# Optimization experiments

Hardware: AMD Instinct MI355X
Metric: run time of the kernel (lower is better)

Reference implementation:

```python
import jax, jax.numpy as jnp
import numpy as np
from jax import lax

F_CNT = 64    # factories per player
U_CNT = 2048  # units per player
GRID = 16     # spatial map side after stride-3 conv on 48x48 board


def conv2d(x, w, b, stride=1, pad=1):
    return lax.conv_general_dilated(x, w, (stride, stride), [(pad, pad), (pad, pad)],
                                    dimension_numbers=('NCHW', 'OIHW', 'NCHW')) + b[None, :, None, None]


def prelu(x, a):
    return jnp.where(x > 0, x, a * x)


def linear(x, w, b):
    return x @ w.T + b


def layernorm(x, g, b, eps=1e-5):
    mu = jnp.mean(x, -1, keepdims=True)
    var = jnp.mean((x - mu) ** 2, -1, keepdims=True)
    return (x - mu) / jnp.sqrt(var + eps) * g + b


def maxpool2(x):
    return lax.reduce_window(x, -jnp.inf, lax.max, (1, 1, 2, 2), (1, 1, 2, 2), 'VALID')


def mha4(f0, u0, f1, u1, fw, fb, uw, ub, lw, lb, num_heads=2, hidden=32):
    # FourSequenceMHAttention: per head, per player, separate Q/K/V linears for
    # factories and units; sequence order is [fac_p0, units_p0, fac_p1, units_p1].
    scale = hidden ** 0.5
    heads = []
    for h in range(num_heads):
        Q, K, V = [], [], []
        for i, (f, u) in enumerate(((f0, u0), (f1, u1))):
            b0 = h * 6 + i * 3
            Q.append(linear(f, fw[b0], fb[b0]))
            K.append(linear(f, fw[b0 + 1], fb[b0 + 1]))
            V.append(linear(f, fw[b0 + 2], fb[b0 + 2]))
            Q.append(linear(u, uw[b0], ub[b0]))
            K.append(linear(u, uw[b0 + 1], ub[b0 + 1]))
            V.append(linear(u, uw[b0 + 2], ub[b0 + 2]))
        Qc = jnp.concatenate(Q, 1)
        Kc = jnp.concatenate(K, 1)
        Vc = jnp.concatenate(V, 1)
        attn = jax.nn.softmax(jnp.einsum('bqd,bkd->bqk', Qc, Kc) / scale, axis=-1)
        heads.append(jnp.einsum('bqk,bkd->bqd', attn, Vc))
    return linear(jnp.concatenate(heads, -1), lw, lb)


def scatter_mask(feat, pos, C):
    # one-hot scatter-add of per-unit features onto the 16x16 grid (batch==1)
    gm = jnp.zeros((GRID, GRID, C), feat.dtype).at[pos[:, 0], pos[:, 1]].add(feat[0])
    return jnp.transpose(gm, (2, 0, 1))[None]  # [1,C,16,16]


def _forward(fl, p0_fac_pos, p0_unit_pos, p1_fac_pos, p1_unit_pos):
    (board, p0_fac_feat, p0_unit_feat, p1_fac_feat, p1_unit_feat,
     sp_w1, sp_b1, sp_a1, sp_w2, sp_b2, sp_a2, sp_w3, sp_b3,
     enc_fac_w, enc_fac_b, enc_unit_w, enc_unit_b, enc_lin_w, enc_lin_b,
     ext_fac_w, ext_fac_b, ext_unit_w, ext_unit_b, ext_lin_w, ext_lin_b, ext_ln_g, ext_ln_b,
     v_w1, v_b1, v_a1, v_w2, v_b2, v_a2, v_lw, v_lb,
     fo_w1, fo_b1, fo_a, fo_w2, fo_b2, ro_w1, ro_b1, ro_a, ro_w2, ro_b2) = fl

    sm = prelu(conv2d(board, sp_w1, sp_b1), sp_a1)
    sm = prelu(conv2d(sm, sp_w2, sp_b2), sp_a2)
    sm = conv2d(sm, sp_w3, sp_b3, stride=3, pad=0)  # [1,24,16,16]

    def gather(pos):
        # per-unit gather of the 24-dim spatial feature at (pos_x, pos_y)
        return jnp.transpose(sm[0][:, pos[:, 0], pos[:, 1]], (1, 0))[None]  # [1,N,24]

    f0 = jnp.concatenate([p0_fac_feat, gather(p0_fac_pos)], -1)    # [1,F,31]
    u0 = jnp.concatenate([p0_unit_feat, gather(p0_unit_pos)], -1)  # [1,U,38]
    f1 = jnp.concatenate([p1_fac_feat, gather(p1_fac_pos)], -1)
    u1 = jnp.concatenate([p1_unit_feat, gather(p1_unit_pos)], -1)

    gmu0 = scatter_mask(p0_unit_feat, p0_unit_pos, 14)
    gmf0 = scatter_mask(p0_fac_feat, p0_fac_pos, 7)
    gmu1 = scatter_mask(p1_unit_feat, p1_unit_pos, 14)
    gmf1 = scatter_mask(p1_fac_feat, p1_fac_pos, 7)
    # loop prepends each team's masks: after p1 order is [u1, f1, u0, f0, spatial]
    v_map = jnp.concatenate([gmu1, gmf1, gmu0, gmf0, sm], 1)  # [1,66,16,16]

    seq = mha4(f0, u0, f1, u1, enc_fac_w, enc_fac_b, enc_unit_w, enc_unit_b, enc_lin_w, enc_lin_b)
    S0, S1, S2 = F_CNT, F_CNT + U_CNT, 2 * F_CNT + U_CNT
    for l in range(2):
        new = mha4(seq[:, :S0], seq[:, S0:S1], seq[:, S1:S2], seq[:, S2:],
                   ext_fac_w[l], ext_fac_b[l], ext_unit_w[l], ext_unit_b[l],
                   ext_lin_w[l], ext_lin_b[l])
        seq = layernorm(seq + new, ext_ln_g[l], ext_ln_b[l])

    def head2(x, w1, b1, a, w2, b2):
        return linear(prelu(linear(x, w1, b1), a), w2, b2)

    f0o = head2(seq[:, :S0], fo_w1, fo_b1, fo_a, fo_w2, fo_b2)      # [1,F,4]
    u0o = head2(seq[:, S0:S1], ro_w1, ro_b1, ro_a, ro_w2, ro_b2)    # [1,U,17]
    f1o = head2(seq[:, S1:S2], fo_w1, fo_b1, fo_a, fo_w2, fo_b2)
    u1o = head2(seq[:, S2:], ro_w1, ro_b1, ro_a, ro_w2, ro_b2)

    vm = maxpool2(prelu(conv2d(v_map, v_w1, v_b1), v_a1))  # [1,96,8,8]
    vm = maxpool2(prelu(conv2d(vm, v_w2, v_b2), v_a2))     # [1,128,4,4]
    v = jnp.tanh(vm.reshape(vm.shape[0], -1) @ v_lw.T + v_lb)  # [1,1]
    return (f0o, u0o, f1o, u1o, v)


def setup_inputs() -> dict:
    key = jax.random.key(0)
    ks = iter(jax.random.split(key, 64))

    def rn(shape, s=1.0):
        return s * jax.random.normal(next(ks), shape, dtype=jnp.float32)

    def ri(shape):
        return jax.random.randint(next(ks), shape, 0, GRID)

    a25 = lambda: jnp.full((1,), 0.25, jnp.float32)  # torch PReLU default
    inp = {
        'board': rn((1, 14, 48, 48)),
        'p0_fac_feat': rn((1, F_CNT, 7)), 'p0_unit_feat': rn((1, U_CNT, 14)),
        'p1_fac_feat': rn((1, F_CNT, 7)), 'p1_unit_feat': rn((1, U_CNT, 14)),
        'sp_w1': rn((48, 14, 3, 3), 0.05), 'sp_b1': rn((48,), 0.05), 'sp_a1': a25(),
        'sp_w2': rn((96, 48, 3, 3), 0.05), 'sp_b2': rn((96,), 0.05), 'sp_a2': a25(),
        'sp_w3': rn((24, 96, 3, 3), 0.05), 'sp_b3': rn((24,), 0.05),
        'enc_fac_w': rn((12, 32, 31), 0.05), 'enc_fac_b': rn((12, 32), 0.05),
        'enc_unit_w': rn((12, 32, 38), 0.05), 'enc_unit_b': rn((12, 32), 0.05),
        'enc_lin_w': rn((32, 64), 0.05), 'enc_lin_b': rn((32,), 0.05),
        'ext_fac_w': rn((2, 12, 32, 32), 0.05), 'ext_fac_b': rn((2, 12, 32), 0.05),
        'ext_unit_w': rn((2, 12, 32, 32), 0.05), 'ext_unit_b': rn((2, 12, 32), 0.05),
        'ext_lin_w': rn((2, 32, 64), 0.05), 'ext_lin_b': rn((2, 32), 0.05),
        'ext_ln_g': jnp.ones((2, 32), jnp.float32), 'ext_ln_b': jnp.zeros((2, 32), jnp.float32),
        'v_w1': rn((96, 66, 3, 3), 0.05), 'v_b1': rn((96,), 0.05), 'v_a1': a25(),
        'v_w2': rn((128, 96, 3, 3), 0.05), 'v_b2': rn((128,), 0.05), 'v_a2': a25(),
        'v_lw': rn((1, 128 * 16), 0.05), 'v_lb': rn((1,), 0.05),
        'fo_w1': rn((32, 32), 0.05), 'fo_b1': rn((32,), 0.05), 'fo_a': a25(),
        'fo_w2': rn((4, 32), 0.05), 'fo_b2': rn((4,), 0.05),
        'ro_w1': rn((32, 32), 0.05), 'ro_b1': rn((32,), 0.05), 'ro_a': a25(),
        'ro_w2': rn((17, 32), 0.05), 'ro_b2': rn((17,), 0.05),
        'p0_fac_pos': ri((F_CNT, 2)), 'p0_unit_pos': ri((U_CNT, 2)),
        'p1_fac_pos': ri((F_CNT, 2)), 'p1_unit_pos': ri((U_CNT, 2)),
    }
    return inp


def reference(board, p0_fac_feat, p0_unit_feat, p1_fac_feat, p1_unit_feat,
              sp_w1, sp_b1, sp_a1, sp_w2, sp_b2, sp_a2, sp_w3, sp_b3,
              enc_fac_w, enc_fac_b, enc_unit_w, enc_unit_b, enc_lin_w, enc_lin_b,
              ext_fac_w, ext_fac_b, ext_unit_w, ext_unit_b, ext_lin_w, ext_lin_b, ext_ln_g, ext_ln_b,
              v_w1, v_b1, v_a1, v_w2, v_b2, v_a2, v_lw, v_lb,
              fo_w1, fo_b1, fo_a, fo_w2, fo_b2, ro_w1, ro_b1, ro_a, ro_w2, ro_b2,
              p0_fac_pos, p0_unit_pos, p1_fac_pos, p1_unit_pos):
    fl = (board, p0_fac_feat, p0_unit_feat, p1_fac_feat, p1_unit_feat,
          sp_w1, sp_b1, sp_a1, sp_w2, sp_b2, sp_a2, sp_w3, sp_b3,
          enc_fac_w, enc_fac_b, enc_unit_w, enc_unit_b, enc_lin_w, enc_lin_b,
          ext_fac_w, ext_fac_b, ext_unit_w, ext_unit_b, ext_lin_w, ext_lin_b, ext_ln_g, ext_ln_b,
          v_w1, v_b1, v_a1, v_w2, v_b2, v_a2, v_lw, v_lb,
          fo_w1, fo_b1, fo_a, fo_w2, fo_b2, ro_w1, ro_b1, ro_a, ro_w2, ro_b2)
    return _forward(fl, p0_fac_pos, p0_unit_pos, p1_fac_pos, p1_unit_pos)
```

## Files before the change

### kernel.cpp

```cpp
#include <hip/hip_runtime.h>
#include <hip/hip_bf16.h>

#define SEQ 4224
typedef unsigned int uint;
typedef unsigned short ushort;
typedef __attribute__((ext_vector_type(8))) short bf16x8;
typedef __attribute__((ext_vector_type(4))) float f32x4;

__device__ __forceinline__ float prelu_f(float x, float a){ return x > 0.f ? x : a*x; }

__device__ __forceinline__ ushort bfr(float x){
  uint u = __float_as_uint(x);
  u = (u + 0x7fffu + ((u>>16)&1u)) >> 16;
  return (ushort)u;
}
__device__ __forceinline__ uint pkbf(float a, float b){
  __hip_bfloat162 h2 = __float22bfloat162_rn(make_float2(a,b));
  union { __hip_bfloat162 h; uint u; } cv; cv.h = h2; return cv.u;
}

#define QSCALE 0.25505607190037247f

template<int CIN, int COUT, int HW, int ACT, int CPT>
__global__ __launch_bounds__(256) void conv3x3_v2(const float* __restrict__ in, const float* __restrict__ w,
                          const float* __restrict__ bias, const float* __restrict__ alpha,
                          float* __restrict__ out) {
  __shared__ float Ws[CPT*CIN*9];
  __shared__ float Bs[CPT];
  const int PXB = HW*HW/256;
  int cg = blockIdx.x / PXB, pxb = blockIdx.x % PXB;
  int tid = threadIdx.x;
  for (int idx=tid; idx<CPT*CIN*9; idx+=256) Ws[idx] = w[cg*CPT*CIN*9 + idx];
  if (tid<CPT) Bs[tid] = bias[cg*CPT+tid];
  __syncthreads();
  int p = pxb*256 + tid;
  int x = p % HW, y = p / HW;
  float a = ACT ? alpha[0] : 0.f;
  float acc[CPT];
  #pragma unroll
  for (int c=0;c<CPT;++c) acc[c]=Bs[c];
  #pragma unroll 2
  for (int i=0;i<CIN;++i){
    const float* ip = in + i*HW*HW;
    float win[9];
    #pragma unroll
    for (int ky=0;ky<3;++ky){
      int yy = y+ky-1;
      #pragma unroll
      for (int kx=0;kx<3;++kx){
        int xx = x+kx-1;
        bool ok = ((unsigned)yy < (unsigned)HW) && ((unsigned)xx < (unsigned)HW);
        win[ky*3+kx] = ok ? ip[yy*HW+xx] : 0.f;
      }
    }
    #pragma unroll
    for (int c=0;c<CPT;++c){
      const float* wp = &Ws[(c*CIN+i)*9];
      #pragma unroll
      for (int k=0;k<9;++k) acc[c] += win[k]*wp[k];
    }
  }
  #pragma unroll
  for (int c=0;c<CPT;++c){
    float v = acc[c];
    if (ACT) v = prelu_f(v, a);
    out[(cg*CPT+c)*HW*HW + p] = v;
  }
}

__global__ __launch_bounds__(256) void conv_s3_v2(const float* __restrict__ in, const float* __restrict__ w,
                        const float* __restrict__ bias, float* __restrict__ out) {
  __shared__ float Ws[2*96*9];
  int cg = blockIdx.x;
  int tid = threadIdx.x;
  for (int idx=tid; idx<1728; idx+=256) Ws[idx] = w[cg*1728 + idx];
  __syncthreads();
  int x = tid&15, y = tid>>4;
  float a0 = bias[2*cg], a1 = bias[2*cg+1];
  const float* ip0 = in + y*144 + x*3;
  #pragma unroll 4
  for (int i=0;i<96;++i){
    const float* ip = ip0 + i*2304;
    float win[9];
    #pragma unroll
    for (int ky=0;ky<3;++ky)
      #pragma unroll
      for (int kx=0;kx<3;++kx) win[ky*3+kx] = ip[ky*48+kx];
    const float* w0 = &Ws[i*9];
    const float* w1 = &Ws[864 + i*9];
    #pragma unroll
    for (int k=0;k<9;++k){ a0 += win[k]*w0[k]; a1 += win[k]*w1[k]; }
  }
  out[(2*cg)*256 + y*16 + x] = a0;
  out[(2*cg+1)*256 + y*16 + x] = a1;
}

__global__ __launch_bounds__(256) void gather_concat(const float* __restrict__ sm,
  const float* __restrict__ p0f, const float* __restrict__ p0u,
  const float* __restrict__ p1f, const float* __restrict__ p1u,
  const int* __restrict__ p0fp, const int* __restrict__ p0up,
  const int* __restrict__ p1fp, const int* __restrict__ p1up,
  float* __restrict__ F0, float* __restrict__ U0, float* __restrict__ F1, float* __restrict__ U1)
{
  int e = blockIdx.x*256+threadIdx.x;
  if (e>=SEQ) return;
  const float* feat; const int* pos; float* dst; int nf, n;
  if (e<64){ n=e; feat=p0f+n*7; pos=p0fp; dst=F0+n*31; nf=7; }
  else if (e<2112){ n=e-64; feat=p0u+n*14; pos=p0up; dst=U0+(size_t)n*38; nf=14; }
  else if (e<2176){ n=e-2112; feat=p1f+n*7; pos=p1fp; dst=F1+n*31; nf=7; }
  else { n=e-2176; feat=p1u+n*14; pos=p1up; dst=U1+(size_t)n*38; nf=14; }
  for (int c=0;c<nf;++c) dst[c]=feat[c];
  int px = pos[2*n], py = pos[2*n+1];
  const float* s = sm + px*16 + py;
  #pragma unroll
  for (int c=0;c<24;++c) dst[nf+c] = s[c*256];
}

__global__ __launch_bounds__(256) void vmap_init(const float* __restrict__ sm, float* __restrict__ vmap){
  int t = blockIdx.x*256+threadIdx.x;
  if (t>=66*256) return;
  int c = t>>8;
  vmap[t] = (c<42)? 0.f : sm[t - 42*256];
}

__global__ __launch_bounds__(256) void vmap_scatter(
  const float* __restrict__ p0f, const float* __restrict__ p0u,
  const float* __restrict__ p1f, const float* __restrict__ p1u,
  const int* __restrict__ p0fp, const int* __restrict__ p0up,
  const int* __restrict__ p1fp, const int* __restrict__ p1up,
  float* __restrict__ vmap)
{
  int e = blockIdx.x*256+threadIdx.x;
  if (e>=SEQ) return;
  const float* feat; const int* pos; int n, ch0, C;
  if (e<2048){ n=e; feat=p1u+n*14; pos=p1up; ch0=0; C=14; }
  else if (e<2112){ n=e-2048; feat=p1f+n*7; pos=p1fp; ch0=14; C=7; }
  else if (e<4160){ n=e-2112; feat=p0u+n*14; pos=p0up; ch0=21; C=14; }
  else { n=e-4160; feat=p0f+n*7; pos=p0fp; ch0=35; C=7; }
  int off = pos[2*n]*16 + pos[2*n+1];
  for (int c=0;c<C;++c) atomicAdd(&vmap[(ch0+c)*256 + off], feat[c]);
}

__global__ __launch_bounds__(256) void qkv_proj2(const float* __restrict__ x0, const float* __restrict__ x1,
    const float* __restrict__ x2, const float* __restrict__ x3, int ind_f, int ind_u,
    const float* __restrict__ fw, const float* __restrict__ fb,
    const float* __restrict__ uw, const float* __restrict__ ub,
    ushort* __restrict__ Q16, ushort* __restrict__ K16, ushort* __restrict__ VT16){
  __shared__ float Xs[64*40];
  __shared__ float Ws[32*40];
  __shared__ float Bs[32];
  int blk = blockIdx.x;
  int chunk = blk % 66;
  int hm = blk / 66;
  int m = hm >> 1, h = hm & 1;
  const float* xb; int ind, isfac, pl;
  if (chunk==0){ xb=x0; ind=ind_f; isfac=1; pl=0; }
  else if (chunk<=32){ xb=x1 + (size_t)(chunk-1)*64*ind_u; ind=ind_u; isfac=0; pl=0; }
  else if (chunk==33){ xb=x2; ind=ind_f; isfac=1; pl=1; }
  else { xb=x3 + (size_t)(chunk-34)*64*ind_u; ind=ind_u; isfac=0; pl=1; }
  int b0 = h*6 + pl*3 + m;
  const float* w = (isfac? fw:uw) + (size_t)b0*32*ind;
  const float* bias = (isfac? fb:ub) + b0*32;
  int tid = threadIdx.x;
  {
    int r = tid>>2, seg = tid&3;
    const float* xr = xb + (size_t)r*ind;
    #pragma unroll
    for (int j=0;j<10;++j){
      int c = seg*10+j;
      Xs[r*40+c] = (c<ind) ? xr[c] : 0.f;
    }
    int o = tid>>3, sg = tid&7;
    const float* wr = w + (size_t)o*ind;
    #pragma unroll
    for (int j=0;j<5;++j){
      int c = sg*5+j;
      Ws[o*40+c] = (c<ind) ? wr[c] : 0.f;
    }
    if (tid<32) Bs[tid]=bias[tid];
  }
  __syncthreads();
  int og = tid&7, rg = tid>>3;
  const float4* Xs4 = (const float4*)Xs;
  const float4* Ws4 = (const float4*)Ws;
  float acc[2][4];
  #pragma unroll
  for (int k=0;k<4;++k){ float b = Bs[og+8*k]; acc[0][k]=b; acc[1][k]=b; }
  #pragma unroll
  for (int d4=0; d4<10; ++d4){
    float4 xa = Xs4[rg*10+d4];
    float4 xb2 = Xs4[(rg+32)*10+d4];
    #pragma unroll
    for (int k=0;k<4;++k){
      float4 wv = Ws4[(og+8*k)*10+d4];
      acc[0][k] += xa.x*wv.x + xa.y*wv.y + xa.z*wv.z + xa.w*wv.w;
      acc[1][k] += xb2.x*wv.x + xb2.y*wv.y + xb2.z*wv.z + xb2.w*wv.w;
    }
  }
  if (m==0){
    #pragma unroll
    for (int j=0;j<2;++j){
      int r = rg + 32*j;
      ushort* base = Q16 + ((size_t)h*SEQ + chunk*64 + r)*32;
      #pragma unroll
      for (int k=0;k<4;++k) base[og+8*k] = bfr(acc[j][k]*QSCALE);
    }
  } else if (m==1){
    #pragma unroll
    for (int j=0;j<2;++j){
      int r = rg + 32*j;
      ushort* base = K16 + ((size_t)h*SEQ + chunk*64 + r)*32;
      #pragma unroll
      for (int k=0;k<4;++k) base[og+8*k] = bfr(acc[j][k]);
    }
  } else {
    #pragma unroll
    for (int k=0;k<4;++k){
      ushort* base = VT16 + ((size_t)h*32 + og+8*k)*SEQ + chunk*64;
      #pragma unroll
      for (int j=0;j<2;++j) base[rg+32*j] = bfr(acc[j][k]);
    }
  }
}

#define KSPLIT 6
#define KITERS 11
__global__ __launch_bounds__(256) void flash_mfma(const ushort* __restrict__ Q16,
    const ushort* __restrict__ K16, const ushort* __restrict__ VT16,
    float* __restrict__ Hpart, float* __restrict__ aux){
  __shared__ ushort Ks[2][64][40];
  __shared__ ushort VTs[2][32][80];
  __shared__ ushort Pl[4][16][72];
  int qb = blockIdx.x, h = blockIdx.y, ks = blockIdx.z;
  int tid = threadIdx.x;
  int wv = tid>>6, l = tid&63, lq = l&15, g = l>>4;
  const ushort* Qh = Q16 + (size_t)h*SEQ*32;
  const ushort* Kh = K16 + (size_t)h*SEQ*32;
  const ushort* VTh = VT16 + (size_t)h*32*SEQ;

  bf16x8 qf = *(const bf16x8*)(Qh + (size_t)(qb*64 + wv*16 + lq)*32 + g*8);

  int krow = tid>>2, kc8 = (tid&3)*8;
  int vd = tid>>3, vk8 = (tid&7)*8;

  f32x4 o0 = {0.f,0.f,0.f,0.f}, o1 = {0.f,0.f,0.f,0.f};
  float mr = -1e30f, lrow = 0.f;

  int kt0 = ks*KITERS;
  bf16x8 kpre = *(const bf16x8*)(Kh + (size_t)(kt0*64 + krow)*32 + kc8);
  bf16x8 vpre = *(const bf16x8*)(VTh + (size_t)vd*SEQ + kt0*64 + vk8);
  *(bf16x8*)&Ks[0][krow][kc8] = kpre;
  *(bf16x8*)&VTs[0][vd][vk8] = vpre;

  for (int it=0; it<KITERS; ++it){
    int pb = it&1;
    if (it+1 < KITERS){
      kpre = *(const bf16x8*)(Kh + (size_t)((kt0+it+1)*64 + krow)*32 + kc8);
      vpre = *(const bf16x8*)(VTh + (size_t)vd*SEQ + (kt0+it+1)*64 + vk8);
    }
    __syncthreads();
    f32x4 z = {0.f,0.f,0.f,0.f};
    f32x4 sT[4];
    #pragma unroll
    for (int m=0;m<4;++m){
      bf16x8 kf = *(const bf16x8*)&Ks[pb][16*m + lq][g*8];
      sT[m] = __builtin_amdgcn_mfma_f32_16x16x32_bf16(kf, qf, z, 0, 0, 0);
    }
    float tm = -1e30f;
    #pragma unroll
    for (int m=0;m<4;++m)
      tm = fmaxf(tm, fmaxf(fmaxf(sT[m][0],sT[m][1]), fmaxf(sT[m][2],sT[m][3])));
    tm = fmaxf(tm, __shfl_xor(tm,16));
    tm = fmaxf(tm, __shfl_xor(tm,32));
    float mnew = fmaxf(mr, tm);
    float rsc = exp2f(mr - mnew);
    float ts = 0.f;
    #pragma unroll
    for (int m=0;m<4;++m){
      #pragma unroll
      for (int r=0;r<4;++r){ float p = exp2f(sT[m][r]-mnew); sT[m][r]=p; ts+=p; }
    }
    ts += __shfl_xor(ts,16); ts += __shfl_xor(ts,32);
    lrow = lrow*rsc + ts; mr = mnew;
    #pragma unroll
    for (int m=0;m<4;++m){
      uint2 pw; pw.x = pkbf(sT[m][0],sT[m][1]); pw.y = pkbf(sT[m][2],sT[m][3]);
      *(uint2*)&Pl[wv][lq][16*m + g*4] = pw;
    }
    float rr0 = __shfl(rsc, (g<<2)+0);
    float rr1 = __shfl(rsc, (g<<2)+1);
    float rr2 = __shfl(rsc, (g<<2)+2);
    float rr3 = __shfl(rsc, (g<<2)+3);
    o0[0]*=rr0; o0[1]*=rr1; o0[2]*=rr2; o0[3]*=rr3;
    o1[0]*=rr0; o1[1]*=rr1; o1[2]*=rr2; o1[3]*=rr3;
    #pragma unroll
    for (int s=0;s<2;++s){
      bf16x8 pf = *(const bf16x8*)&Pl[wv][lq][s*32 + g*8];
      bf16x8 vf0 = *(const bf16x8*)&VTs[pb][lq][s*32 + g*8];
      bf16x8 vf1 = *(const bf16x8*)&VTs[pb][lq+16][s*32 + g*8];
      o0 = __builtin_amdgcn_mfma_f32_16x16x32_bf16(pf, vf0, o0, 0, 0, 0);
      o1 = __builtin_amdgcn_mfma_f32_16x16x32_bf16(pf, vf1, o1, 0, 0, 0);
    }
    if (it+1 < KITERS){
      *(bf16x8*)&Ks[pb^1][krow][kc8] = kpre;
      *(bf16x8*)&VTs[pb^1][vd][vk8] = vpre;
    }
  }
  int qg0 = qb*64 + wv*16;
  #pragma unroll
  for (int r=0;r<4;++r){
    size_t row = (size_t)ks*SEQ + qg0 + g*4 + r;
    Hpart[row*64 + h*32 + lq]      = o0[r];
    Hpart[row*64 + h*32 + lq + 16] = o1[r];
  }
  if (g==0){
    float* ap = aux + ((size_t)(ks*2+h)*SEQ + qg0 + lq)*2;
    ap[0]=mr; ap[1]=lrow;
  }
}

__device__ __forceinline__ float combine_row(const float* __restrict__ Hp,
    const float* __restrict__ aux, int s, int d){
  int hh = d>>5;
  float m[KSPLIT], li[KSPLIT];
  #pragma unroll
  for (int p=0;p<KSPLIT;++p){
    const float* ap = aux + ((size_t)(p*2+hh)*SEQ + s)*2;
    m[p]=ap[0]; li[p]=ap[1];
  }
  float ms = m[0];
  #pragma unroll
  for (int p=1;p<KSPLIT;++p) ms = fmaxf(ms, m[p]);
  float den = 0.f, hv = 0.f;
  #pragma unroll
  for (int p=0;p<KSPLIT;++p){
    float w = exp2f(m[p]-ms);
    den += li[p]*w;
    hv  += Hp[(size_t)p*SEQ*64 + (size_t)s*64 + d]*w;
  }
  return hv/den;
}

__global__ __launch_bounds__(256) void outlin_enc3(const float* __restrict__ Hp,
     const float* __restrict__ aux, const float* __restrict__ lw,
     const float* __restrict__ lb, float* __restrict__ seqout){
  __shared__ float Ls[32*68];
  __shared__ float Hc[8*68];
  int tid=threadIdx.x;
  int s0 = blockIdx.x*8;
  for (int idx=tid; idx<2048; idx+=256){ int o=idx>>6, d=idx&63; Ls[o*68+d]=lw[idx]; }
  for (int idx=tid; idx<512; idx+=256){
    int sl = idx>>6, d = idx&63;
    Hc[sl*68+d] = combine_row(Hp, aux, s0+sl, d);
  }
  __syncthreads();
  int o = tid&31, sl = tid>>5;
  const float4* H4 = (const float4*)&Hc[sl*68];
  const float4* L4 = (const float4*)&Ls[o*68];
  float acc = lb[o];
  #pragma unroll
  for (int d4=0; d4<16; ++d4){
    float4 hv = H4[d4], lv = L4[d4];
    acc += hv.x*lv.x + hv.y*lv.y + hv.z*lv.z + hv.w*lv.w;
  }
  seqout[(s0+sl)*32+o]=acc;
}

__global__ __launch_bounds__(256) void outlin_ln3(const float* __restrict__ Hp,
    const float* __restrict__ aux, const float* __restrict__ lw,
    const float* __restrict__ lb, const float* __restrict__ seqin,
    const float* __restrict__ g, const float* __restrict__ b, float* __restrict__ seqout){
  __shared__ float Ls[32*68];
  __shared__ float Hc[8*68];
  int tid=threadIdx.x;
  int s0 = blockIdx.x*8;
  for (int idx=tid; idx<2048; idx+=256){ int o=idx>>6, d=idx&63; Ls[o*68+d]=lw[idx]; }
  for (int idx=tid; idx<512; idx+=256){
    int sl = idx>>6, d = idx&63;
    Hc[sl*68+d] = combine_row(Hp, aux, s0+sl, d);
  }
  __syncthreads();
  int o = tid&31, sl = tid>>5;
  const float4* H4 = (const float4*)&Hc[sl*68];
  const float4* L4 = (const float4*)&Ls[o*68];
  float acc = lb[o] + seqin[(s0+sl)*32+o];
  #pragma unroll
  for (int d4=0; d4<16; ++d4){
    float4 hv = H4[d4], lv = L4[d4];
    acc += hv.x*lv.x + hv.y*lv.y + hv.z*lv.z + hv.w*lv.w;
  }
  float sum=acc;
  #pragma unroll
  for (int off=1; off<32; off<<=1) sum += __shfl_xor(sum,off);
  float mu = sum*0.03125f;
  float dv = acc-mu;
  float vs = dv*dv;
  #pragma unroll
  for (int off=1; off<32; off<<=1) vs += __shfl_xor(vs,off);
  float rstd = rsqrtf(vs*0.03125f + 1e-5f);
  seqout[(s0+sl)*32+o] = dv*rstd*g[o] + b[o];
}

__global__ __launch_bounds__(256) void head_mlp(const float* __restrict__ seq,
  const float* __restrict__ fw1,const float* __restrict__ fb1,const float* __restrict__ fa,
  const float* __restrict__ fw2,const float* __restrict__ fb2,
  const float* __restrict__ rw1,const float* __restrict__ rb1,const float* __restrict__ ra,
  const float* __restrict__ rw2,const float* __restrict__ rb2,
  float* __restrict__ out)
{
  int e = blockIdx.x*256+threadIdx.x;
  if (e>=SEQ) return;
  const float *w1,*b1,*w2,*b2; float a; int od; float* dst;
  if (e<64){ w1=fw1;b1=fb1;a=fa[0];w2=fw2;b2=fb2;od=4; dst=out + e*4; }
  else if (e<2112){ w1=rw1;b1=rb1;a=ra[0];w2=rw2;b2=rb2;od=17; dst=out + 256 + (size_t)(e-64)*17; }
  else if (e<2176){ w1=fw1;b1=fb1;a=fa[0];w2=fw2;b2=fb2;od=4; dst=out + 35072 + (e-2112)*4; }
  else { w1=rw1;b1=rb1;a=ra[0];w2=rw2;b2=rb2;od=17; dst=out + 35328 + (size_t)(e-2176)*17; }
  float x[32];
  #pragma unroll
  for (int i=0;i<32;++i) x[i]=seq[(size_t)e*32+i];
  float hbuf[32];
  #pragma unroll
  for (int j=0;j<32;++j){
    float acc=b1[j];
    #pragma unroll
    for (int i=0;i<32;++i) acc+=w1[j*32+i]*x[i];
    hbuf[j]=prelu_f(acc,a);
  }
  for (int k=0;k<od;++k){
    float acc=b2[k];
    #pragma unroll
    for (int j=0;j<32;++j) acc+=w2[k*32+j]*hbuf[j];
    dst[k]=acc;
  }
}

__global__ __launch_bounds__(128) void vconv1_pool(const float* __restrict__ in, const float* __restrict__ w,
    const float* __restrict__ bias, const float* __restrict__ alpha, float* __restrict__ out){
  __shared__ float In[66*160];
  __shared__ float Wc[594];
  int c = blockIdx.x >> 1, half = blockIdx.x & 1;
  int y0 = half*8;
  int tid = threadIdx.x;
  const float4* in4 = (const float4*)in;
  float4* In4 = (float4*)In;
  for (int idx4=tid; idx4<2640; idx4+=128){
    int i = idx4/40, rem = idx4 - i*40;
    int r = rem>>2, x4 = rem&3;
    int y = y0 - 1 + r;
    float4 v;
    if ((unsigned)y < 16u) v = in4[i*64 + y*4 + x4];
    else { v.x=v.y=v.z=v.w=0.f; }
    In4[idx4] = v;
  }
  for (int idx=tid; idx<594; idx+=128) Wc[idx] = w[c*594 + idx];
  __syncthreads();
  int x = tid & 15, ry = tid >> 4;
  float a = alpha[0];
  float acc = bias[c];
  for (int i=0;i<66;++i){
    const float* base = &In[i*160 + ry*16];
    const float* wp = &Wc[i*9];
    #pragma unroll
    for (int ky=0;ky<3;++ky){
      const float* row = base + ky*16;
      #pragma unroll
      for (int kx=0;kx<3;++kx){
        int xx = x+kx-1;
        float v = ((unsigned)xx<16u) ? row[xx] : 0.f;
        acc += v*wp[ky*3+kx];
      }
    }
  }
  acc = prelu_f(acc, a);
  float mx = fmaxf(acc, __shfl_xor(acc,1));
  mx = fmaxf(mx, __shfl_xor(mx,16));
  if (((x&1)==0) && ((ry&1)==0))
    out[c*64 + (half*4 + (ry>>1))*8 + (x>>1)] = mx;
}

__global__ __launch_bounds__(64) void vconv2_pool(const float* __restrict__ in, const float* __restrict__ w,
    const float* __restrict__ bias, const float* __restrict__ alpha, float* __restrict__ out){
  __shared__ float In[96*64];
  __shared__ float Ws[864];
  int c = blockIdx.x;
  int tid = threadIdx.x;
  const float4* in4 = (const float4*)in;
  float4* In4 = (float4*)In;
  for (int idx4=tid; idx4<1536; idx4+=64) In4[idx4] = in4[idx4];
  for (int idx=tid; idx<864; idx+=64) Ws[idx] = w[c*864 + idx];
  __syncthreads();
  int x = tid&7, y = tid>>3;
  float acc = bias[c];
  for (int i=0;i<96;++i){
    const float* base = &In[i*64];
    const float* wp = &Ws[i*9];
    #pragma unroll
    for (int ky=0;ky<3;++ky){
      int yy = y+ky-1;
      #pragma unroll
      for (int kx=0;kx<3;++kx){
        int xx = x+kx-1;
        bool ok = ((unsigned)yy<8u) && ((unsigned)xx<8u);
        float v = ok ? base[yy*8+xx] : 0.f;
        acc += v*wp[ky*3+kx];
      }
    }
  }
  acc = prelu_f(acc, alpha[0]);
  float mx = fmaxf(acc, __shfl_xor(acc,1));
  mx = fmaxf(mx, __shfl_xor(mx,8));
  if (((x&1)==0) && ((y&1)==0))
    out[c*16 + (y>>1)*4 + (x>>1)] = mx;
}

__global__ __launch_bounds__(256) void vfinal(const float* __restrict__ vp2, const float* __restrict__ lw,
                       const float* __restrict__ lb, float* __restrict__ outv){
  __shared__ float red[256];
  int tid=threadIdx.x;
  float s=0.f;
  for (int i=tid;i<2048;i+=256) s += vp2[i]*lw[i];
  red[tid]=s; __syncthreads();
  for (int k=128;k>0;k>>=1){ if (tid<k) red[tid]+=red[tid+k]; __syncthreads(); }
  if (tid==0) outv[0] = tanhf(red[0]+lb[0]);
}

extern "C" void kernel_launch(void* const* d_in, const int* in_sizes, int n_in,
                              void* d_out, int out_size, void* d_ws, size_t ws_size,
                              hipStream_t stream){
  (void)in_sizes; (void)n_in; (void)out_size; (void)ws_size;
  const float* board = (const float*)d_in[0];
  const float* p0f = (const float*)d_in[1];
  const float* p0u = (const float*)d_in[2];
  const float* p1f = (const float*)d_in[3];
  const float* p1u = (const float*)d_in[4];
  const float* sp_w1=(const float*)d_in[5];  const float* sp_b1=(const float*)d_in[6];  const float* sp_a1=(const float*)d_in[7];
  const float* sp_w2=(const float*)d_in[8];  const float* sp_b2=(const float*)d_in[9];  const float* sp_a2=(const float*)d_in[10];
  const float* sp_w3=(const float*)d_in[11]; const float* sp_b3=(const float*)d_in[12];
  const float* enc_fac_w=(const float*)d_in[13]; const float* enc_fac_b=(const float*)d_in[14];
  const float* enc_unit_w=(const float*)d_in[15]; const float* enc_unit_b=(const float*)d_in[16];
  const float* enc_lin_w=(const float*)d_in[17]; const float* enc_lin_b=(const float*)d_in[18];
  const float* ext_fac_w=(const float*)d_in[19]; const float* ext_fac_b=(const float*)d_in[20];
  const float* ext_unit_w=(const float*)d_in[21]; const float* ext_unit_b=(const float*)d_in[22];
  const float* ext_lin_w=(const float*)d_in[23]; const float* ext_lin_b=(const float*)d_in[24];
  const float* ext_ln_g=(const float*)d_in[25]; const float* ext_ln_b=(const float*)d_in[26];
  const float* v_w1=(const float*)d_in[27]; const float* v_b1=(const float*)d_in[28]; const float* v_a1=(const float*)d_in[29];
  const float* v_w2=(const float*)d_in[30]; const float* v_b2=(const float*)d_in[31]; const float* v_a2=(const float*)d_in[32];
  const float* v_lw=(const float*)d_in[33]; const float* v_lb=(const float*)d_in[34];
  const float* fo_w1=(const float*)d_in[35]; const float* fo_b1=(const float*)d_in[36]; const float* fo_a=(const float*)d_in[37];
  const float* fo_w2=(const float*)d_in[38]; const float* fo_b2=(const float*)d_in[39];
  const float* ro_w1=(const float*)d_in[40]; const float* ro_b1=(const float*)d_in[41]; const float* ro_a=(const float*)d_in[42];
  const float* ro_w2=(const float*)d_in[43]; const float* ro_b2=(const float*)d_in[44];
  const int* p0fp=(const int*)d_in[45]; const int* p0up=(const int*)d_in[46];
  const int* p1fp=(const int*)d_in[47]; const int* p1up=(const int*)d_in[48];
  float* out = (float*)d_out;

  float* W = (float*)d_ws;
  float* sm1 = W;
  float* sm2 = sm1 + 110592;
  float* sm  = sm2 + 221184;
  float* F0  = sm + 6144;
  float* U0  = F0 + 1984;
  float* F1  = U0 + 77824;
  float* U1  = F1 + 1984;
  ushort* q16 = (ushort*)(U1 + 77824);
  ushort* k16 = q16 + 2*SEQ*32;
  ushort* vt16 = k16 + 2*SEQ*32;
  float* Hp  = (float*)(vt16 + 2*SEQ*32);
  float* aux = Hp + KSPLIT*SEQ*64;
  float* seqA= aux + KSPLIT*2*SEQ*2;
  float* seqB= seqA + SEQ*32;
  float* vmap= seqB + SEQ*32;
  float* vp1 = vmap + 66*256;
  float* vp2 = vp1 + 96*64;

  conv3x3_v2<14,48,48,1,4><<<108,256,0,stream>>>(board, sp_w1, sp_b1, sp_a1, sm1);
  conv3x3_v2<48,96,48,1,4><<<216,256,0,stream>>>(sm1, sp_w2, sp_b2, sp_a2, sm2);
  conv_s3_v2<<<12,256,0,stream>>>(sm2, sp_w3, sp_b3, sm);
  gather_concat<<<17,256,0,stream>>>(sm, p0f,p0u,p1f,p1u, p0fp,p0up,p1fp,p1up, F0,U0,F1,U1);
  vmap_init<<<66,256,0,stream>>>(sm, vmap);
  vmap_scatter<<<17,256,0,stream>>>(p0f,p0u,p1f,p1u, p0fp,p0up,p1fp,p1up, vmap);
  vconv1_pool<<<192,128,0,stream>>>(vmap, v_w1, v_b1, v_a1, vp1);
  vconv2_pool<<<128,64,0,stream>>>(vp1, v_w2, v_b2, v_a2, vp2);
  vfinal<<<1,256,0,stream>>>(vp2, v_lw, v_lb, out + 70144);

  qkv_proj2<<<396,256,0,stream>>>(F0,U0,F1,U1, 31,38, enc_fac_w,enc_fac_b,enc_unit_w,enc_unit_b, q16,k16,vt16);
  flash_mfma<<<dim3(66,2,KSPLIT),256,0,stream>>>(q16,k16,vt16,Hp,aux);
  outlin_enc3<<<528,256,0,stream>>>(Hp, aux, enc_lin_w, enc_lin_b, seqA);
  qkv_proj2<<<396,256,0,stream>>>(seqA, seqA+64*32, seqA+2112*32, seqA+2176*32, 32,32,
      ext_fac_w, ext_fac_b, ext_unit_w, ext_unit_b, q16,k16,vt16);
  flash_mfma<<<dim3(66,2,KSPLIT),256,0,stream>>>(q16,k16,vt16,Hp,aux);
  outlin_ln3<<<528,256,0,stream>>>(Hp, aux, ext_lin_w, ext_lin_b, seqA, ext_ln_g, ext_ln_b, seqB);
  qkv_proj2<<<396,256,0,stream>>>(seqB, seqB+64*32, seqB+2112*32, seqB+2176*32, 32,32,
      ext_fac_w+12288, ext_fac_b+384, ext_unit_w+12288, ext_unit_b+384, q16,k16,vt16);
  flash_mfma<<<dim3(66,2,KSPLIT),256,0,stream>>>(q16,k16,vt16,Hp,aux);
  outlin_ln3<<<528,256,0,stream>>>(Hp, aux, ext_lin_w+2048, ext_lin_b+32, seqB, ext_ln_g+32, ext_ln_b+32, seqA);

  head_mlp<<<17,256,0,stream>>>(seqA, fo_w1,fo_b1,fo_a,fo_w2,fo_b2, ro_w1,ro_b1,ro_a,ro_w2,ro_b2, out);
}
```

Baseline: 405.1 us.

## Fuse whole forward pass into one cooperative persistent megakernel with grid syncs

Replaces the chain of about 19 separate kernel launches with a single cooperative kernel of 512 persistent blocks. The blocks walk every stage as work items and separate stages with grid-wide barriers, so per-launch overhead and inter-kernel gaps go away. The attention key split also changes from 6 to 11 chunks (KITERS 11 to 6), giving more flash work items but more partials to combine. If the cooperative launch fails, it falls back to launching the per-stage kernels separately. Risks are grid-sync cost, occupancy limits from the shared-memory union, and load imbalance on small stages.

New measurement: 1.121 ms. 177% more time.

```diff
diff --git a/kernel.cpp b/kernel.cpp
--- a/kernel.cpp
+++ b/kernel.cpp
@@ -1,7 +1,13 @@
 #include <hip/hip_runtime.h>
 #include <hip/hip_bf16.h>
+#include <hip/hip_cooperative_groups.h>
+
+namespace cg = cooperative_groups;
 
 #define SEQ 4224
+#define KSPLIT 11
+#define KITERS 6
+#define NBLK 512
 typedef unsigned int uint;
 typedef unsigned short ushort;
 typedef __attribute__((ext_vector_type(8))) short bf16x8;
@@ -21,24 +27,36 @@
 
 #define QSCALE 0.25505607190037247f
 
-template<int CIN, int COUT, int HW, int ACT, int CPT>
-__global__ __launch_bounds__(256) void conv3x3_v2(const float* __restrict__ in, const float* __restrict__ w,
-                          const float* __restrict__ bias, const float* __restrict__ alpha,
-                          float* __restrict__ out) {
-  __shared__ float Ws[CPT*CIN*9];
-  __shared__ float Bs[CPT];
-  const int PXB = HW*HW/256;
-  int cg = blockIdx.x / PXB, pxb = blockIdx.x % PXB;
-  int tid = threadIdx.x;
-  for (int idx=tid; idx<CPT*CIN*9; idx+=256) Ws[idx] = w[cg*CPT*CIN*9 + idx];
-  if (tid<CPT) Bs[tid] = bias[cg*CPT+tid];
+struct MegaParams {
+  const float *board,*p0f,*p0u,*p1f,*p1u;
+  const float *sp_w1,*sp_b1,*sp_a1,*sp_w2,*sp_b2,*sp_a2,*sp_w3,*sp_b3;
+  const float *enc_fac_w,*enc_fac_b,*enc_unit_w,*enc_unit_b,*enc_lin_w,*enc_lin_b;
+  const float *ext_fac_w,*ext_fac_b,*ext_unit_w,*ext_unit_b,*ext_lin_w,*ext_lin_b,*ext_ln_g,*ext_ln_b;
+  const float *v_w1,*v_b1,*v_a1,*v_w2,*v_b2,*v_a2,*v_lw,*v_lb;
+  const float *fo_w1,*fo_b1,*fo_a,*fo_w2,*fo_b2,*ro_w1,*ro_b1,*ro_a,*ro_w2,*ro_b2;
+  const int *p0fp,*p0up,*p1fp,*p1up;
+  float* out;
+  float *sm1,*sm2,*sm,*F0,*U0,*F1,*U1;
+  ushort *q16,*k16,*vt16;
+  float *Hp,*aux,*seqA,*seqB,*vmap,*vp1,*vp2;
+};
+
+template<int CIN, int HW>
+__device__ __forceinline__ void conv_item(int cg_, int pxb, int tid,
+    const float* __restrict__ in, const float* __restrict__ w,
+    const float* __restrict__ bias, const float* __restrict__ alpha,
+    float* __restrict__ out, float* SF){
+  float* Ws = SF;
+  float* Bs = SF + 4*CIN*9;
+  for (int idx=tid; idx<4*CIN*9; idx+=256) Ws[idx] = w[cg_*4*CIN*9 + idx];
+  if (tid<4) Bs[tid] = bias[cg_*4+tid];
   __syncthreads();
   int p = pxb*256 + tid;
   int x = p % HW, y = p / HW;
-  float a = ACT ? alpha[0] : 0.f;
-  float acc[CPT];
-  #pragma unroll
-  for (int c=0;c<CPT;++c) acc[c]=Bs[c];
+  float a = alpha[0];
+  float acc[4];
+  #pragma unroll
+  for (int c=0;c<4;++c) acc[c]=Bs[c];
   #pragma unroll 2
   for (int i=0;i<CIN;++i){
     const float* ip = in + i*HW*HW;
@@ -54,29 +72,25 @@
       }
     }
     #pragma unroll
-    for (int c=0;c<CPT;++c){
+    for (int c=0;c<4;++c){
       const float* wp = &Ws[(c*CIN+i)*9];
       #pragma unroll
       for (int k=0;k<9;++k) acc[c] += win[k]*wp[k];
     }
   }
   #pragma unroll
-  for (int c=0;c<CPT;++c){
-    float v = acc[c];
-    if (ACT) v = prelu_f(v, a);
-    out[(cg*CPT+c)*HW*HW + p] = v;
-  }
-}
-
-__global__ __launch_bounds__(256) void conv_s3_v2(const float* __restrict__ in, const float* __restrict__ w,
-                        const float* __restrict__ bias, float* __restrict__ out) {
-  __shared__ float Ws[2*96*9];
-  int cg = blockIdx.x;
-  int tid = threadIdx.x;
-  for (int idx=tid; idx<1728; idx+=256) Ws[idx] = w[cg*1728 + idx];
+  for (int c=0;c<4;++c)
+    out[(cg_*4+c)*HW*HW + p] = prelu_f(acc[c], a);
+}
+
+__device__ __forceinline__ void convs3_item(int cg_, int tid,
+    const float* __restrict__ in, const float* __restrict__ w,
+    const float* __restrict__ bias, float* __restrict__ out, float* SF){
+  float* Ws = SF;
+  for (int idx=tid; idx<1728; idx+=256) Ws[idx] = w[cg_*1728 + idx];
   __syncthreads();
   int x = tid&15, y = tid>>4;
-  float a0 = bias[2*cg], a1 = bias[2*cg+1];
+  float a0 = bias[2*cg_], a1 = bias[2*cg_+1];
   const float* ip0 = in + y*144 + x*3;
   #pragma unroll 4
   for (int i=0;i<96;++i){
@@ -91,65 +105,43 @@
     #pragma unroll
     for (int k=0;k<9;++k){ a0 += win[k]*w0[k]; a1 += win[k]*w1[k]; }
   }
-  out[(2*cg)*256 + y*16 + x] = a0;
-  out[(2*cg+1)*256 + y*16 + x] = a1;
-}
-
-__global__ __launch_bounds__(256) void gather_concat(const float* __restrict__ sm,
-  const float* __restrict__ p0f, const float* __restrict__ p0u,
-  const float* __restrict__ p1f, const float* __restrict__ p1u,
-  const int* __restrict__ p0fp, const int* __restrict__ p0up,
-  const int* __restrict__ p1fp, const int* __restrict__ p1up,
-  float* __restrict__ F0, float* __restrict__ U0, float* __restrict__ F1, float* __restrict__ U1)
-{
-  int e = blockIdx.x*256+threadIdx.x;
+  out[(2*cg_)*256 + y*16 + x] = a0;
+  out[(2*cg_+1)*256 + y*16 + x] = a1;
+}
+
+__device__ __forceinline__ void gather_item(int e, const MegaParams& P){
   if (e>=SEQ) return;
   const float* feat; const int* pos; float* dst; int nf, n;
-  if (e<64){ n=e; feat=p0f+n*7; pos=p0fp; dst=F0+n*31; nf=7; }
-  else if (e<2112){ n=e-64; feat=p0u+n*14; pos=p0up; dst=U0+(size_t)n*38; nf=14; }
-  else if (e<2176){ n=e-2112; feat=p1f+n*7; pos=p1fp; dst=F1+n*31; nf=7; }
-  else { n=e-2176; feat=p1u+n*14; pos=p1up; dst=U1+(size_t)n*38; nf=14; }
+  if (e<64){ n=e; feat=P.p0f+n*7; pos=P.p0fp; dst=P.F0+n*31; nf=7; }
+  else if (e<2112){ n=e-64; feat=P.p0u+n*14; pos=P.p0up; dst=P.U0+(size_t)n*38; nf=14; }
+  else if (e<2176){ n=e-2112; feat=P.p1f+n*7; pos=P.p1fp; dst=P.F1+n*31; nf=7; }
+  else { n=e-2176; feat=P.p1u+n*14; pos=P.p1up; dst=P.U1+(size_t)n*38; nf=14; }
   for (int c=0;c<nf;++c) dst[c]=feat[c];
   int px = pos[2*n], py = pos[2*n+1];
-  const float* s = sm + px*16 + py;
+  const float* s = P.sm + px*16 + py;
   #pragma unroll
   for (int c=0;c<24;++c) dst[nf+c] = s[c*256];
 }
 
-__global__ __launch_bounds__(256) void vmap_init(const float* __restrict__ sm, float* __restrict__ vmap){
-  int t = blockIdx.x*256+threadIdx.x;
-  if (t>=66*256) return;
-  int c = t>>8;
-  vmap[t] = (c<42)? 0.f : sm[t - 42*256];
-}
-
-__global__ __launch_bounds__(256) void vmap_scatter(
-  const float* __restrict__ p0f, const float* __restrict__ p0u,
-  const float* __restrict__ p1f, const float* __restrict__ p1u,
-  const int* __restrict__ p0fp, const int* __restrict__ p0up,
-  const int* __restrict__ p1fp, const int* __restrict__ p1up,
-  float* __restrict__ vmap)
-{
-  int e = blockIdx.x*256+threadIdx.x;
+__device__ __forceinline__ void scatter_item(int e, const MegaParams& P){
   if (e>=SEQ) return;
   const float* feat; const int* pos; int n, ch0, C;
-  if (e<2048){ n=e; feat=p1u+n*14; pos=p1up; ch0=0; C=14; }
-  else if (e<2112){ n=e-2048; feat=p1f+n*7; pos=p1fp; ch0=14; C=7; }
-  else if (e<4160){ n=e-2112; feat=p0u+n*14; pos=p0up; ch0=21; C=14; }
-  else { n=e-4160; feat=p0f+n*7; pos=p0fp; ch0=35; C=7; }
+  if (e<2048){ n=e; feat=P.p1u+n*14; pos=P.p1up; ch0=0; C=14; }
+  else if (e<2112){ n=e-2048; feat=P.p1f+n*7; pos=P.p1fp; ch0=14; C=7; }
+  else if (e<4160){ n=e-2112; feat=P.p0u+n*14; pos=P.p0up; ch0=21; C=14; }
+  else { n=e-4160; feat=P.p0f+n*7; pos=P.p0fp; ch0=35; C=7; }
   int off = pos[2*n]*16 + pos[2*n+1];
-  for (int c=0;c<C;++c) atomicAdd(&vmap[(ch0+c)*256 + off], feat[c]);
-}
-
-__global__ __launch_bounds__(256) void qkv_proj2(const float* __restrict__ x0, const float* __restrict__ x1,
-    const float* __restrict__ x2, const float* __restrict__ x3, int ind_f, int ind_u,
-    const float* __restrict__ fw, const float* __restrict__ fb,
-    const float* __restrict__ uw, const float* __restrict__ ub,
-    ushort* __restrict__ Q16, ushort* __restrict__ K16, ushort* __restrict__ VT16){
-  __shared__ float Xs[64*40];
-  __shared__ float Ws[32*40];
-  __shared__ float Bs[32];
-  int blk = blockIdx.x;
+  for (int c=0;c<C;++c) atomicAdd(&P.vmap[(ch0+c)*256 + off], feat[c]);
+}
+
+__device__ __forceinline__ void qkv_item(int blk, int tid,
+    const float* x0, const float* x1, const float* x2, const float* x3,
+    int ind_f, int ind_u,
+    const float* fw, const float* fb, const float* uw, const float* ub,
+    ushort* Q16, ushort* K16, ushort* VT16, float* SF){
+  float* Xs = SF;
+  float* Ws = SF + 2560;
+  float* Bs = SF + 3840;
   int chunk = blk % 66;
   int hm = blk / 66;
   int m = hm >> 1, h = hm & 1;
@@ -161,22 +153,15 @@
   int b0 = h*6 + pl*3 + m;
   const float* w = (isfac? fw:uw) + (size_t)b0*32*ind;
   const float* bias = (isfac? fb:ub) + b0*32;
-  int tid = threadIdx.x;
   {
     int r = tid>>2, seg = tid&3;
     const float* xr = xb + (size_t)r*ind;
     #pragma unroll
-    for (int j=0;j<10;++j){
-      int c = seg*10+j;
-      Xs[r*40+c] = (c<ind) ? xr[c] : 0.f;
-    }
+    for (int j=0;j<10;++j){ int c = seg*10+j; Xs[r*40+c] = (c<ind) ? xr[c] : 0.f; }
     int o = tid>>3, sg = tid&7;
     const float* wr = w + (size_t)o*ind;
     #pragma unroll
-    for (int j=0;j<5;++j){
-      int c = sg*5+j;
-      Ws[o*40+c] = (c<ind) ? wr[c] : 0.f;
-    }
+    for (int j=0;j<5;++j){ int c = sg*5+j; Ws[o*40+c] = (c<ind) ? wr[c] : 0.f; }
     if (tid<32) Bs[tid]=bias[tid];
   }
   __syncthreads();
@@ -223,16 +208,13 @@
   }
 }
 
-#define KSPLIT 6
-#define KITERS 11
-__global__ __launch_bounds__(256) void flash_mfma(const ushort* __restrict__ Q16,
-    const ushort* __restrict__ K16, const ushort* __restrict__ VT16,
-    float* __restrict__ Hpart, float* __restrict__ aux){
-  __shared__ ushort Ks[2][64][40];
-  __shared__ ushort VTs[2][32][80];
-  __shared__ ushort Pl[4][16][72];
-  int qb = blockIdx.x, h = blockIdx.y, ks = blockIdx.z;
-  int tid = threadIdx.x;
+__device__ __forceinline__ void flash_item(int item, int tid,
+    const ushort* Q16, const ushort* K16, const ushort* VT16,
+    float* Hpart, float* aux, ushort* SU){
+  ushort* KsB = SU;
+  ushort* VTB = SU + 5120;
+  ushort* PlB = SU + 10240;
+  int qb = item % 66, h = (item/66)&1, ks = item/132;
   int wv = tid>>6, l = tid&63, lq = l&15, g = l>>4;
   const ushort* Qh = Q16 + (size_t)h*SEQ*32;
   const ushort* Kh = K16 + (size_t)h*SEQ*32;
@@ -249,8 +231,8 @@
   int kt0 = ks*KITERS;
   bf16x8 kpre = *(const bf16x8*)(Kh + (size_t)(kt0*64 + krow)*32 + kc8);
   bf16x8 vpre = *(const bf16x8*)(VTh + (size_t)vd*SEQ + kt0*64 + vk8);
-  *(bf16x8*)&Ks[0][krow][kc8] = kpre;
-  *(bf16x8*)&VTs[0][vd][vk8] = vpre;
+  *(bf16x8*)&KsB[0*2560 + krow*40 + kc8] = kpre;
+  *(bf16x8*)&VTB[0*2560 + vd*80 + vk8] = vpre;
 
   for (int it=0; it<KITERS; ++it){
     int pb = it&1;
@@ -263,7 +245,7 @@
     f32x4 sT[4];
     #pragma unroll
     for (int m=0;m<4;++m){
-      bf16x8 kf = *(const bf16x8*)&Ks[pb][16*m + lq][g*8];
+      bf16x8 kf = *(const bf16x8*)&KsB[pb*2560 + (16*m+lq)*40 + g*8];
       sT[m] = __builtin_amdgcn_mfma_f32_16x16x32_bf16(kf, qf, z, 0, 0, 0);
     }
     float tm = -1e30f;
@@ -285,7 +267,7 @@
     #pragma unroll
     for (int m=0;m<4;++m){
       uint2 pw; pw.x = pkbf(sT[m][0],sT[m][1]); pw.y = pkbf(sT[m][2],sT[m][3]);
-      *(uint2*)&Pl[wv][lq][16*m + g*4] = pw;
+      *(uint2*)&PlB[wv*1152 + lq*72 + 16*m + g*4] = pw;
     }
     float rr0 = __shfl(rsc, (g<<2)+0);
     float rr1 = __shfl(rsc, (g<<2)+1);
@@ -295,15 +277,15 @@
     o1[0]*=rr0; o1[1]*=rr1; o1[2]*=rr2; o1[3]*=rr3;
     #pragma unroll
     for (int s=0;s<2;++s){
-      bf16x8 pf = *(const bf16x8*)&Pl[wv][lq][s*32 + g*8];
-      bf16x8 vf0 = *(const bf16x8*)&VTs[pb][lq][s*32 + g*8];
-      bf16x8 vf1 = *(const bf16x8*)&VTs[pb][lq+16][s*32 + g*8];
+      bf16x8 pf = *(const bf16x8*)&PlB[wv*1152 + lq*72 + s*32 + g*8];
+      bf16x8 vf0 = *(const bf16x8*)&VTB[pb*2560 + lq*80 + s*32 + g*8];
+      bf16x8 vf1 = *(const bf16x8*)&VTB[pb*2560 + (lq+16)*80 + s*32 + g*8];
       o0 = __builtin_amdgcn_mfma_f32_16x16x32_bf16(pf, vf0, o0, 0, 0, 0);
       o1 = __builtin_amdgcn_mfma_f32_16x16x32_bf16(pf, vf1, o1, 0, 0, 0);
     }
     if (it+1 < KITERS){
-      *(bf16x8*)&Ks[pb^1][krow][kc8] = kpre;
-      *(bf16x8*)&VTs[pb^1][vd][vk8] = vpre;
+      *(bf16x8*)&KsB[(pb^1)*2560 + krow*40 + kc8] = kpre;
+      *(bf16x8*)&VTB[(pb^1)*2560 + vd*80 + vk8] = vpre;
     }
   }
   int qg0 = qb*64 + wv*16;
@@ -319,8 +301,7 @@
   }
 }
 
-__device__ __forceinline__ float combine_row(const float* __restrict__ Hp,
-    const float* __restrict__ aux, int s, int d){
+__device__ __forceinline__ float combine_row(const float* Hp, const float* aux, int s, int d){
   int hh = d>>5;
   float m[KSPLIT], li[KSPLIT];
   #pragma unroll
@@ -341,13 +322,13 @@
   return hv/den;
 }
 
-__global__ __launch_bounds__(256) void outlin_enc3(const float* __restrict__ Hp,
-     const float* __restrict__ aux, const float* __restrict__ lw,
-     const float* __restrict__ lb, float* __restrict__ seqout){
-  __shared__ float Ls[32*68];
-  __shared__ float Hc[8*68];
-  int tid=threadIdx.x;
-  int s0 = blockIdx.x*8;
+__device__ __forceinline__ void outlin_item(int blk, int tid,
+    const float* Hp, const float* aux, const float* lw, const float* lb,
+    const float* seqin, const float* g, const float* b, float* seqout,
+    bool LN, float* SF){
+  float* Ls = SF;
+  float* Hc = SF + 2176;
+  int s0 = blk*8;
   for (int idx=tid; idx<2048; idx+=256){ int o=idx>>6, d=idx&63; Ls[o*68+d]=lw[idx]; }
   for (int idx=tid; idx<512; idx+=256){
     int sl = idx>>6, d = idx&63;
@@ -357,94 +338,57 @@
   int o = tid&31, sl = tid>>5;
   const float4* H4 = (const float4*)&Hc[sl*68];
   const float4* L4 = (const float4*)&Ls[o*68];
-  float acc = lb[o];
+  float acc = lb[o] + (LN ? seqin[(s0+sl)*32+o] : 0.f);
   #pragma unroll
   for (int d4=0; d4<16; ++d4){
     float4 hv = H4[d4], lv = L4[d4];
     acc += hv.x*lv.x + hv.y*lv.y + hv.z*lv.z + hv.w*lv.w;
   }
-  seqout[(s0+sl)*32+o]=acc;
-}
-
-__global__ __launch_bounds__(256) void outlin_ln3(const float* __restrict__ Hp,
-    const float* __restrict__ aux, const float* __restrict__ lw,
-    const float* __restrict__ lb, const float* __restrict__ seqin,
-    const float* __restrict__ g, const float* __restrict__ b, float* __restrict__ seqout){
-  __shared__ float Ls[32*68];
-  __shared__ float Hc[8*68];
-  int tid=threadIdx.x;
-  int s0 = blockIdx.x*8;
-  for (int idx=tid; idx<2048; idx+=256){ int o=idx>>6, d=idx&63; Ls[o*68+d]=lw[idx]; }
-  for (int idx=tid; idx<512; idx+=256){
-    int sl = idx>>6, d = idx&63;
-    Hc[sl*68+d] = combine_row(Hp, aux, s0+sl, d);
-  }
-  __syncthreads();
-  int o = tid&31, sl = tid>>5;
-  const float4* H4 = (const float4*)&Hc[sl*68];
-  const float4* L4 = (const float4*)&Ls[o*68];
-  float acc = lb[o] + seqin[(s0+sl)*32+o];
-  #pragma unroll
-  for (int d4=0; d4<16; ++d4){
-    float4 hv = H4[d4], lv = L4[d4];
-    acc += hv.x*lv.x + hv.y*lv.y + hv.z*lv.z + hv.w*lv.w;
-  }
-  float sum=acc;
-  #pragma unroll
-  for (int off=1; off<32; off<<=1) sum += __shfl_xor(sum,off);
-  float mu = sum*0.03125f;
-  float dv = acc-mu;
-  float vs = dv*dv;
-  #pragma unroll
-  for (int off=1; off<32; off<<=1) vs += __shfl_xor(vs,off);
-  float rstd = rsqrtf(vs*0.03125f + 1e-5f);
-  seqout[(s0+sl)*32+o] = dv*rstd*g[o] + b[o];
-}
-
-__global__ __launch_bounds__(256) void head_mlp(const float* __restrict__ seq,
-  const float* __restrict__ fw1,const float* __restrict__ fb1,const float* __restrict__ fa,
-  const float* __restrict__ fw2,const float* __restrict__ fb2,
-  const float* __restrict__ rw1,const float* __restrict__ rb1,const float* __restrict__ ra,
-  const float* __restrict__ rw2,const float* __restrict__ rb2,
-  float* __restrict__ out)
-{
-  int e = blockIdx.x*256+threadIdx.x;
-  if (e>=SEQ) return;
-  const float *w1,*b1,*w2,*b2; float a; int od; float* dst;
-  if (e<64){ w1=fw1;b1=fb1;a=fa[0];w2=fw2;b2=fb2;od=4; dst=out + e*4; }
-  else if (e<2112){ w1=rw1;b1=rb1;a=ra[0];w2=rw2;b2=rb2;od=17; dst=out + 256 + (size_t)(e-64)*17; }
-  else if (e<2176){ w1=fw1;b1=fb1;a=fa[0];w2=fw2;b2=fb2;od=4; dst=out + 35072 + (e-2112)*4; }
-  else { w1=rw1;b1=rb1;a=ra[0];w2=rw2;b2=rb2;od=17; dst=out + 35328 + (size_t)(e-2176)*17; }
-  float x[32];
-  #pragma unroll
-  for (int i=0;i<32;++i) x[i]=seq[(size_t)e*32+i];
-  float hbuf[32];
-  #pragma unroll
-  for (int j=0;j<32;++j){
-    float acc=b1[j];
-    #pragma unroll
-    for (int i=0;i<32;++i) acc+=w1[j*32+i]*x[i];
-    hbuf[j]=prelu_f(acc,a);
-  }
-  for (int k=0;k<od;++k){
-    float acc=b2[k];
-    #pragma unroll
-    for (int j=0;j<32;++j) acc+=w2[k*32+j]*hbuf[j];
-    dst[k]=acc;
-  }
-}
-
-__global__ __launch_bounds__(128) void vconv1_pool(const float* __restrict__ in, const float* __restrict__ w,
-    const float* __restrict__ bias, const float* __restrict__ alpha, float* __restrict__ out){
-  __shared__ float In[66*160];
-  __shared__ float Wc[594];
-  int c = blockIdx.x >> 1, half = blockIdx.x & 1;
-  int y0 = half*8;
-  int tid = threadIdx.x;
-  const float4* in4 = (const float4*)in;
+  if (LN){
+    float sum=acc;
+    #pragma unroll
+    for (int off=1; off<32; off<<=1) sum += __shfl_xor(sum,off);
+    float mu = sum*0.03125f;
+    float dv = acc-mu;
+    float vs = dv*dv;
+    #pragma unroll
+    for (int off=1; off<32; off<<=1) vs += __shfl_xor(vs,off);
+    float rstd = rsqrtf(vs*0.03125f + 1e-5f);
+    seqout[(s0+sl)*32+o] = dv*rstd*g[o] + b[o];
+  } else {
+    seqout[(s0+sl)*32+o] = acc;
+  }
+}
+
+__device__ __forceinline__ void qkv_layer(const MegaParams& P, int layer, int blk, int tid, float* SF){
+  if (layer==0)
+    qkv_item(blk, tid, P.F0,P.U0,P.F1,P.U1, 31,38,
+        P.enc_fac_w,P.enc_fac_b,P.enc_unit_w,P.enc_unit_b, P.q16,P.k16,P.vt16, SF);
+  else if (layer==1)
+    qkv_item(blk, tid, P.seqA, P.seqA+64*32, P.seqA+2112*32, P.seqA+2176*32, 32,32,
+        P.ext_fac_w,P.ext_fac_b,P.ext_unit_w,P.ext_unit_b, P.q16,P.k16,P.vt16, SF);
+  else
+    qkv_item(blk, tid, P.seqB, P.seqB+64*32, P.seqB+2112*32, P.seqB+2176*32, 32,32,
+        P.ext_fac_w+12288,P.ext_fac_b+384,P.ext_unit_w+12288,P.ext_unit_b+384, P.q16,P.k16,P.vt16, SF);
+}
+__device__ __forceinline__ void outlin_layer(const MegaParams& P, int layer, int blk, int tid, float* SF){
+  if (layer==0)
+    outlin_item(blk,tid,P.Hp,P.aux,P.enc_lin_w,P.enc_lin_b,nullptr,nullptr,nullptr,P.seqA,false,SF);
+  else if (layer==1)
+    outlin_item(blk,tid,P.Hp,P.aux,P.ext_lin_w,P.ext_lin_b,P.seqA,P.ext_ln_g,P.ext_ln_b,P.seqB,true,SF);
+  else
+    outlin_item(blk,tid,P.Hp,P.aux,P.ext_lin_w+2048,P.ext_lin_b+32,P.seqB,P.ext_ln_g+32,P.ext_ln_b+32,P.seqA,true,SF);
+}
+
+__device__ __forceinline__ void vconv1_item(int item2, int tid, const MegaParams& P, float* SF){
+  float* In = SF;
+  float* Wc = SF + 6336;
+  int c = item2>>2, q = item2&3;
+  int y0 = q*4;
+  const float4* in4 = (const float4*)P.vmap;
   float4* In4 = (float4*)In;
-  for (int idx4=tid; idx4<2640; idx4+=128){
-    int i = idx4/40, rem = idx4 - i*40;
+  for (int idx4=tid; idx4<1584; idx4+=256){
+    int i = idx4/24, rem = idx4 - i*24;
     int r = rem>>2, x4 = rem&3;
     int y = y0 - 1 + r;
     float4 v;
@@ -452,148 +396,299 @@
     else { v.x=v.y=v.z=v.w=0.f; }
     In4[idx4] = v;
   }
-  for (int idx=tid; idx<594; idx+=128) Wc[idx] = w[c*594 + idx];
+  for (int idx=tid; idx<594; idx+=256) Wc[idx] = P.v_w1[c*594 + idx];
   __syncthreads();
-  int x = tid & 15, ry = tid >> 4;
-  float a = alpha[0];
-  float acc = bias[c];
-  for (int i=0;i<66;++i){
-    const float* base = &In[i*160 + ry*16];
-    const float* wp = &Wc[i*9];
-    #pragma unroll
-    for (int ky=0;ky<3;++ky){
-      const float* row = base + ky*16;
-      #pragma unroll
-      for (int kx=0;kx<3;++kx){
-        int xx = x+kx-1;
-        float v = ((unsigned)xx<16u) ? row[xx] : 0.f;
-        acc += v*wp[ky*3+kx];
+  if (tid<64){
+    int x = tid & 15, ry = tid >> 4;
+    float a = P.v_a1[0];
+    float acc = P.v_b1[c];
+    for (int i=0;i<66;++i){
+      const float* base = &In[i*96 + ry*16];
+      const float* wp = &Wc[i*9];
+      #pragma unroll
+      for (int ky=0;ky<3;++ky){
+        const float* row = base + ky*16;
+        #pragma unroll
+        for (int kx=0;kx<3;++kx){
+          int xx = x+kx-1;
+          float v = ((unsigned)xx<16u) ? row[xx] : 0.f;
+          acc += v*wp[ky*3+kx];
+        }
       }
     }
-  }
-  acc = prelu_f(acc, a);
-  float mx = fmaxf(acc, __shfl_xor(acc,1));
-  mx = fmaxf(mx, __shfl_xor(mx,16));
-  if (((x&1)==0) && ((ry&1)==0))
-    out[c*64 + (half*4 + (ry>>1))*8 + (x>>1)] = mx;
-}
-
-__global__ __launch_bounds__(64) void vconv2_pool(const float* __restrict__ in, const float* __restrict__ w,
-    const float* __restrict__ bias, const float* __restrict__ alpha, float* __restrict__ out){
-  __shared__ float In[96*64];
-  __shared__ float Ws[864];
-  int c = blockIdx.x;
-  int tid = threadIdx.x;
-  const float4* in4 = (const float4*)in;
+    acc = prelu_f(acc, a);
+    float mx = fmaxf(acc, __shfl_xor(acc,1));
+    mx = fmaxf(mx, __shfl_xor(mx,16));
+    if (((x&1)==0) && ((ry&1)==0))
+      P.vp1[c*64 + (q*2 + (ry>>1))*8 + (x>>1)] = mx;
+  }
+}
+
+__device__ __forceinline__ void vconv2_item(int c, int tid, const MegaParams& P, float* SF){
+  float* In = SF;
+  float* Ws = SF + 6144;
+  const float4* in4 = (const float4*)P.vp1;
   float4* In4 = (float4*)In;
-  for (int idx4=tid; idx4<1536; idx4+=64) In4[idx4] = in4[idx4];
-  for (int idx=tid; idx<864; idx+=64) Ws[idx] = w[c*864 + idx];
+  for (int idx4=tid; idx4<1536; idx4+=256) In4[idx4] = in4[idx4];
+  for (int idx=tid; idx<864; idx+=256) Ws[idx] = P.v_w2[c*864 + idx];
   __syncthreads();
-  int x = tid&7, y = tid>>3;
-  float acc = bias[c];
-  for (int i=0;i<96;++i){
-    const float* base = &In[i*64];
-    const float* wp = &Ws[i*9];
-    #pragma unroll
-    for (int ky=0;ky<3;++ky){
-      int yy = y+ky-1;
-      #pragma unroll
-      for (int kx=0;kx<3;++kx){
-        int xx = x+kx-1;
-        bool ok = ((unsigned)yy<8u) && ((unsigned)xx<8u);
-        float v = ok ? base[yy*8+xx] : 0.f;
-        acc += v*wp[ky*3+kx];
+  if (tid<64){
+    int x = tid&7, y = tid>>3;
+    float acc = P.v_b2[c];
+    for (int i=0;i<96;++i){
+      const float* base = &In[i*64];
+      const float* wp = &Ws[i*9];
+      #pragma unroll
+      for (int ky=0;ky<3;++ky){
+        int yy = y+ky-1;
+        #pragma unroll
+        for (int kx=0;kx<3;++kx){
+          int xx = x+kx-1;
+          bool ok = ((unsigned)yy<8u) && ((unsigned)xx<8u);
+          float v = ok ? base[yy*8+xx] : 0.f;
+          acc += v*wp[ky*3+kx];
+        }
       }
     }
-  }
-  acc = prelu_f(acc, alpha[0]);
-  float mx = fmaxf(acc, __shfl_xor(acc,1));
-  mx = fmaxf(mx, __shfl_xor(mx,8));
-  if (((x&1)==0) && ((y&1)==0))
-    out[c*16 + (y>>1)*4 + (x>>1)] = mx;
-}
-
-__global__ __launch_bounds__(256) void vfinal(const float* __restrict__ vp2, const float* __restrict__ lw,
-                       const float* __restrict__ lb, float* __restrict__ outv){
-  __shared__ float red[256];
-  int tid=threadIdx.x;
+    acc = prelu_f(acc, P.v_a2[0]);
+    float mx = fmaxf(acc, __shfl_xor(acc,1));
+    mx = fmaxf(mx, __shfl_xor(mx,8));
+    if (((x&1)==0) && ((y&1)==0))
+      P.vp2[c*16 + (y>>1)*4 + (x>>1)] = mx;
+  }
+}
+
+__device__ __forceinline__ void vfinal_item(int tid, const MegaParams& P, float* SF){
+  float* red = SF;
   float s=0.f;
-  for (int i=tid;i<2048;i+=256) s += vp2[i]*lw[i];
+  for (int i=tid;i<2048;i+=256) s += P.vp2[i]*P.v_lw[i];
   red[tid]=s; __syncthreads();
   for (int k=128;k>0;k>>=1){ if (tid<k) red[tid]+=red[tid+k]; __syncthreads(); }
-  if (tid==0) outv[0] = tanhf(red[0]+lb[0]);
-}
+  if (tid==0) P.out[70144] = tanhf(red[0]+P.v_lb[0]);
+}
+
+__device__ __forceinline__ void head_item(int e, const MegaParams& P){
+  if (e>=SEQ) return;
+  const float *w1,*b1,*w2,*b2; float a; int od; float* dst;
+  float* out = P.out;
+  if (e<64){ w1=P.fo_w1;b1=P.fo_b1;a=P.fo_a[0];w2=P.fo_w2;b2=P.fo_b2;od=4; dst=out + e*4; }
+  else if (e<2112){ w1=P.ro_w1;b1=P.ro_b1;a=P.ro_a[0];w2=P.ro_w2;b2=P.ro_b2;od=17; dst=out + 256 + (size_t)(e-64)*17; }
+  else if (e<2176){ w1=P.fo_w1;b1=P.fo_b1;a=P.fo_a[0];w2=P.fo_w2;b2=P.fo_b2;od=4; dst=out + 35072 + (e-2112)*4; }
+  else { w1=P.ro_w1;b1=P.ro_b1;a=P.ro_a[0];w2=P.ro_w2;b2=P.ro_b2;od=17; dst=out + 35328 + (size_t)(e-2176)*17; }
+  float x[32];
+  #pragma unroll
+  for (int i=0;i<32;++i) x[i]=P.seqA[(size_t)e*32+i];
+  float hbuf[32];
+  #pragma unroll
+  for (int j=0;j<32;++j){
+    float acc=b1[j];
+    #pragma unroll
+    for (int i=0;i<32;++i) acc+=w1[j*32+i]*x[i];
+    hbuf[j]=prelu_f(acc,a);
+  }
+  for (int k=0;k<od;++k){
+    float acc=b2[k];
+    #pragma unroll
+    for (int j=0;j<32;++j) acc+=w2[k*32+j]*hbuf[j];
+    dst[k]=acc;
+  }
+}
+
+__global__ __launch_bounds__(256,2) void mega(MegaParams P){
+  cg::grid_group grid = cg::this_grid();
+  __shared__ __align__(16) char SMEMRAW[29696];
+  float* SF = (float*)SMEMRAW;
+  ushort* SU = (ushort*)SMEMRAW;
+  int tid = threadIdx.x;
+  const int NB = gridDim.x;
+
+  for (int item=blockIdx.x; item<150; item+=NB){
+    __syncthreads();
+    if (item<108) conv_item<14,48>(item/9, item%9, tid, P.board, P.sp_w1, P.sp_b1, P.sp_a1, P.sm1, SF);
+    else P.vmap[(item-108)*256+tid] = 0.f;
+  }
+  grid.sync();
+  for (int item=blockIdx.x; item<216; item+=NB){
+    __syncthreads();
+    conv_item<48,48>(item/9, item%9, tid, P.sm1, P.sp_w2, P.sp_b2, P.sp_a2, P.sm2, SF);
+  }
+  grid.sync();
+  for (int item=blockIdx.x; item<12; item+=NB){
+    __syncthreads();
+    convs3_item(item, tid, P.sm2, P.sp_w3, P.sp_b3, P.sm, SF);
+  }
+  grid.sync();
+  for (int item=blockIdx.x; item<58; item+=NB){
+    if (item<17) gather_item(item*256+tid, P);
+    else if (item<41){ int idx=(item-17)*256+tid; P.vmap[42*256+idx] = P.sm[idx]; }
+    else scatter_item((item-41)*256+tid, P);
+  }
+  grid.sync();
+  for (int item=blockIdx.x; item<780; item+=NB){
+    __syncthreads();
+    if (item<396) qkv_layer(P, 0, item, tid, SF);
+    else vconv1_item(item-396, tid, P, SF);
+  }
+  grid.sync();
+  for (int item=blockIdx.x; item<1580; item+=NB){
+    __syncthreads();
+    if (item<1452) flash_item(item, tid, P.q16,P.k16,P.vt16, P.Hp, P.aux, SU);
+    else vconv2_item(item-1452, tid, P, SF);
+  }
+  grid.sync();
+  for (int item=blockIdx.x; item<529; item+=NB){
+    __syncthreads();
+    if (item<528) outlin_layer(P, 0, item, tid, SF);
+    else vfinal_item(tid, P, SF);
+  }
+  grid.sync();
+  for (int item=blockIdx.x; item<396; item+=NB){
+    __syncthreads();
+    qkv_layer(P, 1, item, tid, SF);
+  }
+  grid.sync();
+  for (int item=blockIdx.x; item<1452; item+=NB){
+    __syncthreads();
+    flash_item(item, tid, P.q16,P.k16,P.vt16, P.Hp, P.aux, SU);
+  }
+  grid.sync();
+  for (int item=blockIdx.x; item<528; item+=NB){
+    __syncthreads();
+    outlin_layer(P, 1, item, tid, SF);
+  }
+  grid.sync();
+  for (int item=blockIdx.x; item<396; item+=NB){
+    __syncthreads();
+    qkv_layer(P, 2, item, tid, SF);
+  }
+  grid.sync();
+  for (int item=blockIdx.x; item<1452; item+=NB){
+    __syncthreads();
+    flash_item(item, tid, P.q16,P.k16,P.vt16, P.Hp, P.aux, SU);
+  }
+  grid.sync();
+  for (int item=blockIdx.x; item<528; item+=NB){
+    __syncthreads();
+    outlin_layer(P, 2, item, tid, SF);
+  }
+  grid.sync();
+  for (int item=blockIdx.x; item<17; item+=NB)
+    head_item(item*256+tid, P);
+}
+
+__global__ __launch_bounds__(256) void k_conv1(MegaParams P){
+  __shared__ __align__(16) float SF[512];
+  conv_item<14,48>(blockIdx.x/9, blockIdx.x%9, threadIdx.x, P.board,P.sp_w1,P.sp_b1,P.sp_a1,P.sm1,SF);
+}
+__global__ __launch_bounds__(256) void k_conv2(MegaParams P){
+  __shared__ __align__(16) float SF[1736];
+  conv_item<48,48>(blockIdx.x/9, blockIdx.x%9, threadIdx.x, P.sm1,P.sp_w2,P.sp_b2,P.sp_a2,P.sm2,SF);
+}
+__global__ __launch_bounds__(256) void k_convs3(MegaParams P){
+  __shared__ __align__(16) float SF[1728];
+  convs3_item(blockIdx.x, threadIdx.x, P.sm2,P.sp_w3,P.sp_b3,P.sm,SF);
+}
+__global__ __launch_bounds__(256) void k_gather(MegaParams P){ gather_item(blockIdx.x*256+threadIdx.x, P); }
+__global__ __launch_bounds__(256) void k_vmapinit(MegaParams P){
+  int t=blockIdx.x*256+threadIdx.x; int c=t>>8;
+  P.vmap[t] = (c<42)?0.f:P.sm[t-42*256];
+}
+__global__ __launch_bounds__(256) void k_scatter(MegaParams P){ scatter_item(blockIdx.x*256+threadIdx.x, P); }
+__global__ __launch_bounds__(256) void k_vconv1(MegaParams P){
+  __shared__ __align__(16) float SF[6930];
+  vconv1_item(blockIdx.x, threadIdx.x, P, SF);
+}
+__global__ __launch_bounds__(256) void k_vconv2(MegaParams P){
+  __shared__ __align__(16) float SF[7008];
+  vconv2_item(blockIdx.x, threadIdx.x, P, SF);
+}
+__global__ __launch_bounds__(256) void k_vfinal(MegaParams P){
+  __shared__ __align__(16) float SF[256];
+  vfinal_item(threadIdx.x, P, SF);
+}
+__global__ __launch_bounds__(256) void k_qkv(MegaParams P, int layer){
+  __shared__ __align__(16) float SF[3904];
+  qkv_layer(P, layer, blockIdx.x, threadIdx.x, SF);
+}
+__global__ __launch_bounds__(256) void k_flash(MegaParams P){
+  __shared__ __align__(16) char SM[29696];
+  flash_item(blockIdx.x, threadIdx.x, P.q16,P.k16,P.vt16,P.Hp,P.aux,(ushort*)SM);
+}
+__global__ __launch_bounds__(256) void k_outlin(MegaParams P, int layer){
+  __shared__ __align__(16) float SF[2720];
+  outlin_layer(P, layer, blockIdx.x, threadIdx.x, SF);
+}
+__global__ __launch_bounds__(256) void k_head(MegaParams P){ head_item(blockIdx.x*256+threadIdx.x, P); }
 
 extern "C" void kernel_launch(void* const* d_in, const int* in_sizes, int n_in,
                               void* d_out, int out_size, void* d_ws, size_t ws_size,
                               hipStream_t stream){
   (void)in_sizes; (void)n_in; (void)out_size; (void)ws_size;
-  const float* board = (const float*)d_in[0];
-  const float* p0f = (const float*)d_in[1];
-  const float* p0u = (const float*)d_in[2];
-  const float* p1f = (const float*)d_in[3];
-  const float* p1u = (const float*)d_in[4];
-  const float* sp_w1=(const float*)d_in[5];  const float* sp_b1=(const float*)d_in[6];  const float* sp_a1=(const float*)d_in[7];
-  const float* sp_w2=(const float*)d_in[8];  const float* sp_b2=(const float*)d_in[9];  const float* sp_a2=(const float*)d_in[10];
-  const float* sp_w3=(const float*)d_in[11]; const float* sp_b3=(const float*)d_in[12];
-  const float* enc_fac_w=(const float*)d_in[13]; const float* enc_fac_b=(const float*)d_in[14];
-  const float* enc_unit_w=(const float*)d_in[15]; const float* enc_unit_b=(const float*)d_in[16];
-  const float* enc_lin_w=(const float*)d_in[17]; const float* enc_lin_b=(const float*)d_in[18];
-  const float* ext_fac_w=(const float*)d_in[19]; const float* ext_fac_b=(const float*)d_in[20];
-  const float* ext_unit_w=(const float*)d_in[21]; const float* ext_unit_b=(const float*)d_in[22];
-  const float* ext_lin_w=(const float*)d_in[23]; const float* ext_lin_b=(const float*)d_in[24];
-  const float* ext_ln_g=(const float*)d_in[25]; const float* ext_ln_b=(const float*)d_in[26];
-  const float* v_w1=(const float*)d_in[27]; const float* v_b1=(const float*)d_in[28]; const float* v_a1=(const float*)d_in[29];
-  const float* v_w2=(const float*)d_in[30]; const float* v_b2=(const float*)d_in[31]; const float* v_a2=(const float*)d_in[32];
-  const float* v_lw=(const float*)d_in[33]; const float* v_lb=(const float*)d_in[34];
-  const float* fo_w1=(const float*)d_in[35]; const float* fo_b1=(const float*)d_in[36]; const float* fo_a=(const float*)d_in[37];
-  const float* fo_w2=(const float*)d_in[38]; const float* fo_b2=(const float*)d_in[39];
-  const float* ro_w1=(const float*)d_in[40]; const float* ro_b1=(const float*)d_in[41]; const float* ro_a=(const float*)d_in[42];
-  const float* ro_w2=(const float*)d_in[43]; const float* ro_b2=(const float*)d_in[44];
-  const int* p0fp=(const int*)d_in[45]; const int* p0up=(const int*)d_in[46];
-  const int* p1fp=(const int*)d_in[47]; const int* p1up=(const int*)d_in[48];
-  float* out = (float*)d_out;
+  MegaParams P;
+  P.board=(const float*)d_in[0];
+  P.p0f=(const float*)d_in[1]; P.p0u=(const float*)d_in[2];
+  P.p1f=(const float*)d_in[3]; P.p1u=(const float*)d_in[4];
+  P.sp_w1=(const float*)d_in[5]; P.sp_b1=(const float*)d_in[6]; P.sp_a1=(const float*)d_in[7];
+  P.sp_w2=(const float*)d_in[8]; P.sp_b2=(const float*)d_in[9]; P.sp_a2=(const float*)d_in[10];
+  P.sp_w3=(const float*)d_in[11]; P.sp_b3=(const float*)d_in[12];
+  P.enc_fac_w=(const float*)d_in[13]; P.enc_fac_b=(const float*)d_in[14];
+  P.enc_unit_w=(const float*)d_in[15]; P.enc_unit_b=(const float*)d_in[16];
+  P.enc_lin_w=(const float*)d_in[17]; P.enc_lin_b=(const float*)d_in[18];
+  P.ext_fac_w=(const float*)d_in[19]; P.ext_fac_b=(const float*)d_in[20];
+  P.ext_unit_w=(const float*)d_in[21]; P.ext_unit_b=(const float*)d_in[22];
+  P.ext_lin_w=(const float*)d_in[23]; P.ext_lin_b=(const float*)d_in[24];
+  P.ext_ln_g=(const float*)d_in[25]; P.ext_ln_b=(const float*)d_in[26];
+  P.v_w1=(const float*)d_in[27]; P.v_b1=(const float*)d_in[28]; P.v_a1=(const float*)d_in[29];
+  P.v_w2=(const float*)d_in[30]; P.v_b2=(const float*)d_in[31]; P.v_a2=(const float*)d_in[32];
+  P.v_lw=(const float*)d_in[33]; P.v_lb=(const float*)d_in[34];
+  P.fo_w1=(const float*)d_in[35]; P.fo_b1=(const float*)d_in[36]; P.fo_a=(const float*)d_in[37];
+  P.fo_w2=(const float*)d_in[38]; P.fo_b2=(const float*)d_in[39];
+  P.ro_w1=(const float*)d_in[40]; P.ro_b1=(const float*)d_in[41]; P.ro_a=(const float*)d_in[42];
+  P.ro_w2=(const float*)d_in[43]; P.ro_b2=(const float*)d_in[44];
+  P.p0fp=(const int*)d_in[45]; P.p0up=(const int*)d_in[46];
+  P.p1fp=(const int*)d_in[47]; P.p1up=(const int*)d_in[48];
+  P.out = (float*)d_out;
 
   float* W = (float*)d_ws;
-  float* sm1 = W;
-  float* sm2 = sm1 + 110592;
-  float* sm  = sm2 + 221184;
-  float* F0  = sm + 6144;
-  float* U0  = F0 + 1984;
-  float* F1  = U0 + 77824;
-  float* U1  = F1 + 1984;
-  ushort* q16 = (ushort*)(U1 + 77824);
-  ushort* k16 = q16 + 2*SEQ*32;
-  ushort* vt16 = k16 + 2*SEQ*32;
-  float* Hp  = (float*)(vt16 + 2*SEQ*32);
-  float* aux = Hp + KSPLIT*SEQ*64;
-  float* seqA= aux + KSPLIT*2*SEQ*2;
-  float* seqB= seqA + SEQ*32;
-  float* vmap= seqB + SEQ*32;
-  float* vp1 = vmap + 66*256;
-  float* vp2 = vp1 + 96*64;
-
-  conv3x3_v2<14,48,48,1,4><<<108,256,0,stream>>>(board, sp_w1, sp_b1, sp_a1, sm1);
-  conv3x3_v2<48,96,48,1,4><<<216,256,0,stream>>>(sm1, sp_w2, sp_b2, sp_a2, sm2);
-  conv_s3_v2<<<12,256,0,stream>>>(sm2, sp_w3, sp_b3, sm);
-  gather_concat<<<17,256,0,stream>>>(sm, p0f,p0u,p1f,p1u, p0fp,p0up,p1fp,p1up, F0,U0,F1,U1);
-  vmap_init<<<66,256,0,stream>>>(sm, vmap);
-  vmap_scatter<<<17,256,0,stream>>>(p0f,p0u,p1f,p1u, p0fp,p0up,p1fp,p1up, vmap);
-  vconv1_pool<<<192,128,0,stream>>>(vmap, v_w1, v_b1, v_a1, vp1);
-  vconv2_pool<<<128,64,0,stream>>>(vp1, v_w2, v_b2, v_a2, vp2);
-  vfinal<<<1,256,0,stream>>>(vp2, v_lw, v_lb, out + 70144);
-
-  qkv_proj2<<<396,256,0,stream>>>(F0,U0,F1,U1, 31,38, enc_fac_w,enc_fac_b,enc_unit_w,enc_unit_b, q16,k16,vt16);
-  flash_mfma<<<dim3(66,2,KSPLIT),256,0,stream>>>(q16,k16,vt16,Hp,aux);
-  outlin_enc3<<<528,256,0,stream>>>(Hp, aux, enc_lin_w, enc_lin_b, seqA);
-  qkv_proj2<<<396,256,0,stream>>>(seqA, seqA+64*32, seqA+2112*32, seqA+2176*32, 32,32,
-      ext_fac_w, ext_fac_b, ext_unit_w, ext_unit_b, q16,k16,vt16);
-  flash_mfma<<<dim3(66,2,KSPLIT),256,0,stream>>>(q16,k16,vt16,Hp,aux);
-  outlin_ln3<<<528,256,0,stream>>>(Hp, aux, ext_lin_w, ext_lin_b, seqA, ext_ln_g, ext_ln_b, seqB);
-  qkv_proj2<<<396,256,0,stream>>>(seqB, seqB+64*32, seqB+2112*32, seqB+2176*32, 32,32,
-      ext_fac_w+12288, ext_fac_b+384, ext_unit_w+12288, ext_unit_b+384, q16,k16,vt16);
-  flash_mfma<<<dim3(66,2,KSPLIT),256,0,stream>>>(q16,k16,vt16,Hp,aux);
-  outlin_ln3<<<528,256,0,stream>>>(Hp, aux, ext_lin_w+2048, ext_lin_b+32, seqB, ext_ln_g+32, ext_ln_b+32, seqA);
-
-  head_mlp<<<17,256,0,stream>>>(seqA, fo_w1,fo_b1,fo_a,fo_w2,fo_b2, ro_w1,ro_b1,ro_a,ro_w2,ro_b2, out);
-}
+  P.sm1 = W;
+  P.sm2 = P.sm1 + 110592;
+  P.sm  = P.sm2 + 221184;
+  P.F0  = P.sm + 6144;
+  P.U0  = P.F0 + 1984;
+  P.F1  = P.U0 + 77824;
+  P.U1  = P.F1 + 1984;
+  P.q16 = (ushort*)(P.U1 + 77824);
+  P.k16 = P.q16 + 2*SEQ*32;
+  P.vt16 = P.k16 + 2*SEQ*32;
+  P.Hp  = (float*)(P.vt16 + 2*SEQ*32);
+  P.aux = P.Hp + KSPLIT*SEQ*64;
+  P.seqA= P.aux + KSPLIT*2*SEQ*2;
+  P.seqB= P.seqA + SEQ*32;
+  P.vmap= P.seqB + SEQ*32;
+  P.vp1 = P.vmap + 66*256;
+  P.vp2 = P.vp1 + 96*64;
+
+  void* kargs[] = { (void*)&P };
+  hipError_t err = hipLaunchCooperativeKernel((const void*)mega, dim3(NBLK), dim3(256), kargs, 0, stream);
+  if (err != hipSuccess){
+    k_conv1<<<108,256,0,stream>>>(P);
+    k_conv2<<<216,256,0,stream>>>(P);
+    k_convs3<<<12,256,0,stream>>>(P);
+    k_gather<<<17,256,0,stream>>>(P);
+    k_vmapinit<<<66,256,0,stream>>>(P);
+    k_scatter<<<17,256,0,stream>>>(P);
+    k_vconv1<<<384,256,0,stream>>>(P);
+    k_vconv2<<<128,256,0,stream>>>(P);
+    k_vfinal<<<1,256,0,stream>>>(P);
+    k_qkv<<<396,256,0,stream>>>(P,0);
+    k_flash<<<1452,256,0,stream>>>(P);
+    k_outlin<<<528,256,0,stream>>>(P,0);
+    k_qkv<<<396,256,0,stream>>>(P,1);
+    k_flash<<<1452,256,0,stream>>>(P);
+    k_outlin<<<528,256,0,stream>>>(P,1);
+    k_qkv<<<396,256,0,stream>>>(P,2);
+    k_flash<<<1452,256,0,stream>>>(P);
+    k_outlin<<<528,256,0,stream>>>(P,2);
+    k_head<<<17,256,0,stream>>>(P);
+  }
+}
```
